# Kernel optimization log

Hardware: AMD Instinct MI355X
Metric: run time of the kernel (lower is better)

## Reference

```python
import jax, jax.numpy as jnp
import numpy as np

TOP_K = 2  # module default top_k


def setup_inputs() -> dict:
    key = jax.random.key(0)
    k1, k2, k3 = jax.random.split(key, 3)
    B, D, E = 4096, 1024, 64  # tokens, input_dim, num_experts
    return {
        "tensor1": jax.random.normal(k1, (B, D), dtype=jnp.float32),
        "tensor2": jax.random.normal(k2, (B, D), dtype=jnp.float32),
        "gate_weight": jax.random.normal(k3, (E, 2 * D), dtype=jnp.float32) * 0.02,
    }


def reference(tensor1, tensor2, gate_weight):
    # x: (B, 2D)
    x = jnp.concatenate((tensor1, tensor2), axis=-1)
    # pairwise L2 distance between each token and each expert vector
    diff = gate_weight[None, :, :] - x[:, None, :]          # (B, E, 2D)
    logits = -jnp.sqrt(jnp.sum(diff * diff, axis=-1))        # (B, E)
    topk_logits, indices = jax.lax.top_k(logits, TOP_K)      # (B, K)
    gating_weights = jax.nn.softmax(topk_logits, axis=-1)    # (B, K)
    rows = jnp.arange(logits.shape[0])[:, None]              # (B, 1)
    sparse_gating = jnp.zeros_like(logits).at[rows, indices].set(gating_weights)
    return sparse_gating
```

## Files before the change

kernel.cpp:

```cpp
#include <hip/hip_runtime.h>
#include <math.h>

#define NTOK 4096
#define NDIM 1024
#define KTOT 2048
#define NEXP 64
#define NKC  8
#define KCH  (KTOT / NKC)
#define NSTEP (KCH / 32)

typedef _Float16 half8 __attribute__((ext_vector_type(8)));
typedef float    floatx4 __attribute__((ext_vector_type(4)));

#define XSCALE 16.0f
#define WSCALE 1024.0f
#define INVSCALE (1.0f / (16.0f * 1024.0f))

struct h2pair { _Float16 h, l; };
__device__ __forceinline__ h2pair split2(float v) {
    h2pair r;
    r.h = (_Float16)v;
    r.l = (_Float16)(v - (float)r.h);
    return r;
}

__global__ __launch_bounds__(256) void prep_w(const float* __restrict__ W,
                                              _Float16* __restrict__ WhT,
                                              _Float16* __restrict__ WlT,
                                              float* __restrict__ nrm) {
    const int e = blockIdx.x, t = threadIdx.x;
    const float* row = W + (size_t)e * KTOT + t * 8;
    const float4 a = *reinterpret_cast<const float4*>(row);
    const float4 b = *reinterpret_cast<const float4*>(row + 4);
    float ss = fmaf(a.x, a.x, fmaf(a.y, a.y, fmaf(a.z, a.z, fmaf(a.w, a.w, 0.f))));
    ss = fmaf(b.x, b.x, fmaf(b.y, b.y, fmaf(b.z, b.z, fmaf(b.w, b.w, ss))));

    const h2pair p0 = split2(a.x * WSCALE), p1 = split2(a.y * WSCALE);
    const h2pair p2 = split2(a.z * WSCALE), p3 = split2(a.w * WSCALE);
    const h2pair p4 = split2(b.x * WSCALE), p5 = split2(b.y * WSCALE);
    const h2pair p6 = split2(b.z * WSCALE), p7 = split2(b.w * WSCALE);
    half8 h, l;
    h[0]=p0.h; h[1]=p1.h; h[2]=p2.h; h[3]=p3.h; h[4]=p4.h; h[5]=p5.h; h[6]=p6.h; h[7]=p7.h;
    l[0]=p0.l; l[1]=p1.l; l[2]=p2.l; l[3]=p3.l; l[4]=p4.l; l[5]=p5.l; l[6]=p6.l; l[7]=p7.l;
    const size_t idx = ((size_t)t * NEXP + e) * 8;
    *reinterpret_cast<half8*>(WhT + idx) = h;
    *reinterpret_cast<half8*>(WlT + idx) = l;

    #pragma unroll
    for (int off = 32; off > 0; off >>= 1) ss += __shfl_down(ss, off, 64);
    __shared__ float red[4];
    const int lane = t & 63, wv = t >> 6;
    if (lane == 0) red[wv] = ss;
    __syncthreads();
    if (t == 0) nrm[e] = (red[0] + red[1]) + (red[2] + red[3]);
}

__global__ __launch_bounds__(256) void gemm_frag(const float* __restrict__ t1,
                                                 const float* __restrict__ t2,
                                                 const _Float16* __restrict__ WhT,
                                                 const _Float16* __restrict__ WlT,
                                                 float* __restrict__ Gp,
                                                 float* __restrict__ Cp) {
    const int tid  = threadIdx.x;
    const int lane = tid & 63;
    const int gw   = blockIdx.x * 4 + (tid >> 6);
    const int tokg = gw >> 3;
    const int kc   = gw & 7;
    const int tok0 = tokg * 16;
    const int kbase = kc * KCH;
    const int n  = lane & 15;
    const int fq = lane >> 4;

    const float* __restrict__ xb = ((kbase < NDIM)
        ? (t1 + (size_t)(tok0 + n) * NDIM + kbase)
        : (t2 + (size_t)(tok0 + n) * NDIM + (kbase - NDIM))) + fq * 8;
    const _Float16* __restrict__ whb = WhT + ((size_t)(kbase >> 3) + fq) * (NEXP * 8) + n * 8;
    const _Float16* __restrict__ wlb = WlT + ((size_t)(kbase >> 3) + fq) * (NEXP * 8) + n * 8;

    floatx4 acc[4];
    #pragma unroll
    for (int j = 0; j < 4; ++j) { acc[j][0]=0.f; acc[j][1]=0.f; acc[j][2]=0.f; acc[j][3]=0.f; }
    float ssx = 0.f;

    #pragma unroll
    for (int s = 0; s < NSTEP; ++s) {
        const float4 x0 = *reinterpret_cast<const float4*>(xb + s * 32);
        const float4 x1 = *reinterpret_cast<const float4*>(xb + s * 32 + 4);
        half8 bh[4], bl[4];
        #pragma unroll
        for (int j = 0; j < 4; ++j) {
            bh[j] = *reinterpret_cast<const half8*>(whb + (size_t)s * 4 * (NEXP * 8) + j * 128);
            bl[j] = *reinterpret_cast<const half8*>(wlb + (size_t)s * 4 * (NEXP * 8) + j * 128);
        }
        ssx = fmaf(x0.x, x0.x, fmaf(x0.y, x0.y, fmaf(x0.z, x0.z, fmaf(x0.w, x0.w, ssx))));
        ssx = fmaf(x1.x, x1.x, fmaf(x1.y, x1.y, fmaf(x1.z, x1.z, fmaf(x1.w, x1.w, ssx))));
        const h2pair q0 = split2(x0.x * XSCALE), q1 = split2(x0.y * XSCALE);
        const h2pair q2 = split2(x0.z * XSCALE), q3 = split2(x0.w * XSCALE);
        const h2pair q4 = split2(x1.x * XSCALE), q5 = split2(x1.y * XSCALE);
        const h2pair q6 = split2(x1.z * XSCALE), q7 = split2(x1.w * XSCALE);
        half8 ah, al;
        ah[0]=q0.h; ah[1]=q1.h; ah[2]=q2.h; ah[3]=q3.h; ah[4]=q4.h; ah[5]=q5.h; ah[6]=q6.h; ah[7]=q7.h;
        al[0]=q0.l; al[1]=q1.l; al[2]=q2.l; al[3]=q3.l; al[4]=q4.l; al[5]=q5.l; al[6]=q6.l; al[7]=q7.l;
        #pragma unroll
        for (int j = 0; j < 4; ++j)
            acc[j] = __builtin_amdgcn_mfma_f32_16x16x32_f16(ah, bh[j], acc[j], 0, 0, 0);
        #pragma unroll
        for (int j = 0; j < 4; ++j)
            acc[j] = __builtin_amdgcn_mfma_f32_16x16x32_f16(al, bh[j], acc[j], 0, 0, 0);
        #pragma unroll
        for (int j = 0; j < 4; ++j)
            acc[j] = __builtin_amdgcn_mfma_f32_16x16x32_f16(ah, bl[j], acc[j], 0, 0, 0);
    }

    #pragma unroll
    for (int j = 0; j < 4; ++j) {
        #pragma unroll
        for (int i = 0; i < 4; ++i) {
            Gp[((size_t)kc * NTOK + tok0 + fq * 4 + i) * NEXP + 16 * j + n] = acc[j][i];
        }
    }

    ssx += __shfl_xor(ssx, 16, 64);
    ssx += __shfl_xor(ssx, 32, 64);
    if (lane < 16)
        Cp[(size_t)kc * NTOK + tok0 + lane] = ssx;
}

__global__ __launch_bounds__(256) void finalize(const float* __restrict__ Gp,
                                                const float* __restrict__ Cp,
                                                const float* __restrict__ nrm,
                                                float* __restrict__ out) {
    const int wv = threadIdx.x >> 6, lane = threadIdx.x & 63;
    const int token = blockIdx.x * 4 + wv;

    float gsum = 0.f, csum = 0.f;
    #pragma unroll
    for (int cix = 0; cix < NKC; ++cix) {
        gsum += Gp[((size_t)cix * NTOK + token) * NEXP + lane];
        csum += Cp[(size_t)cix * NTOK + token];
    }
    const float nv = nrm[lane];

    const float S = fmaf(-2.f * INVSCALE, gsum, csum) + nv;
    const float logit = -sqrtf(S);

    float v1 = logit; int i1 = lane;
    #pragma unroll
    for (int off = 32; off > 0; off >>= 1) {
        float ov = __shfl_xor(v1, off, 64);
        int   oi = __shfl_xor(i1, off, 64);
        if (ov > v1 || (ov == v1 && oi < i1)) { v1 = ov; i1 = oi; }
    }
    float v2 = (lane == i1) ? -__builtin_inff() : logit;
    int   i2 = lane;
    #pragma unroll
    for (int off = 32; off > 0; off >>= 1) {
        float ov = __shfl_xor(v2, off, 64);
        int   oi = __shfl_xor(i2, off, 64);
        if (ov > v2 || (ov == v2 && oi < i2)) { v2 = ov; i2 = oi; }
    }
    const float e2  = expf(v2 - v1);
    const float inv = 1.f / (1.f + e2);
    const float o = (lane == i1) ? inv : ((lane == i2) ? e2 * inv : 0.f);
    out[(size_t)token * NEXP + lane] = o;
}

extern "C" void kernel_launch(void* const* d_in, const int* in_sizes, int n_in,
                              void* d_out, int out_size, void* d_ws, size_t ws_size,
                              hipStream_t stream) {
    const float* t1 = (const float*)d_in[0];
    const float* t2 = (const float*)d_in[1];
    const float* W  = (const float*)d_in[2];
    float* out = (float*)d_out;

    char* ws = (char*)d_ws;
    float*    Gp  = (float*)ws;
    float*    Cp  = Gp + (size_t)NKC * NTOK * NEXP;
    float*    nrm = Cp + (size_t)NKC * NTOK;
    _Float16* WhT = (_Float16*)(nrm + NEXP);
    _Float16* WlT = WhT + (size_t)NEXP * KTOT;

    prep_w<<<NEXP, 256, 0, stream>>>(W, WhT, WlT, nrm);
    gemm_frag<<<(NTOK / 16) * NKC / 4, 256, 0, stream>>>(t1, t2, WhT, WlT, Gp, Cp);
    finalize<<<NTOK / 4, 256, 0, stream>>>(Gp, Cp, nrm, out);
}
```

Measured before the change: 89.96 us.

## Fuse split-K GEMM and top-k finalize into one kernel via LDS reduction

Merges the split-K fragment GEMM and the finalize kernel. Each 512-thread block now handles 16 tokens, with 8 waves each covering one K chunk. Partial dot products and norms go to shared memory (padded stride) instead of global workspace, then are reduced in-block before top-2 softmax. This removes the partial-sum global traffic (8x4096x64 floats written and re-read) and one kernel launch. In exchange the grid has fewer blocks (256), each carrying more LDS.

```diff
diff --git a/kernel.cpp b/kernel.cpp
--- a/kernel.cpp
+++ b/kernel.cpp
@@ -5,9 +5,10 @@
 #define NDIM 1024
 #define KTOT 2048
 #define NEXP 64
-#define NKC  8
-#define KCH  (KTOT / NKC)
+#define NWAVE 8
+#define KCH  (KTOT / NWAVE)
 #define NSTEP (KCH / 32)
+#define RS   68
 
 typedef _Float16 half8 __attribute__((ext_vector_type(8)));
 typedef float    floatx4 __attribute__((ext_vector_type(4)));
@@ -55,19 +56,20 @@
     if (t == 0) nrm[e] = (red[0] + red[1]) + (red[2] + red[3]);
 }
 
-__global__ __launch_bounds__(256) void gemm_frag(const float* __restrict__ t1,
-                                                 const float* __restrict__ t2,
-                                                 const _Float16* __restrict__ WhT,
-                                                 const _Float16* __restrict__ WlT,
-                                                 float* __restrict__ Gp,
-                                                 float* __restrict__ Cp) {
+__global__ __launch_bounds__(512) void gate_fused(const float* __restrict__ t1,
+                                                  const float* __restrict__ t2,
+                                                  const _Float16* __restrict__ WhT,
+                                                  const _Float16* __restrict__ WlT,
+                                                  const float* __restrict__ nrm,
+                                                  float* __restrict__ out) {
+    __shared__ float Sd[NWAVE][16 * RS];
+    __shared__ float Cn[NWAVE][16];
+
     const int tid  = threadIdx.x;
     const int lane = tid & 63;
-    const int gw   = blockIdx.x * 4 + (tid >> 6);
-    const int tokg = gw >> 3;
-    const int kc   = gw & 7;
-    const int tok0 = tokg * 16;
-    const int kbase = kc * KCH;
+    const int wv   = tid >> 6;
+    const int tok0 = blockIdx.x * 16;
+    const int kbase = wv * KCH;
     const int n  = lane & 15;
     const int fq = lane >> 4;
 
@@ -115,54 +117,46 @@
     #pragma unroll
     for (int j = 0; j < 4; ++j) {
         #pragma unroll
-        for (int i = 0; i < 4; ++i) {
-            Gp[((size_t)kc * NTOK + tok0 + fq * 4 + i) * NEXP + 16 * j + n] = acc[j][i];
-        }
+        for (int i = 0; i < 4; ++i)
+            Sd[wv][(fq * 4 + i) * RS + 16 * j + n] = acc[j][i];
     }
-
     ssx += __shfl_xor(ssx, 16, 64);
     ssx += __shfl_xor(ssx, 32, 64);
-    if (lane < 16)
-        Cp[(size_t)kc * NTOK + tok0 + lane] = ssx;
-}
+    if (lane < 16) Cn[wv][lane] = ssx;
+    __syncthreads();
 
-__global__ __launch_bounds__(256) void finalize(const float* __restrict__ Gp,
-                                                const float* __restrict__ Cp,
-                                                const float* __restrict__ nrm,
-                                                float* __restrict__ out) {
-    const int wv = threadIdx.x >> 6, lane = threadIdx.x & 63;
-    const int token = blockIdx.x * 4 + wv;
+    #pragma unroll
+    for (int tt = 0; tt < 2; ++tt) {
+        const int t = wv * 2 + tt;
+        float gsum = 0.f, csum = 0.f;
+        #pragma unroll
+        for (int w = 0; w < NWAVE; ++w) {
+            gsum += Sd[w][t * RS + lane];
+            csum += Cn[w][t];
+        }
+        const float S = fmaf(-2.f * INVSCALE, gsum, csum) + nrm[lane];
+        const float logit = -sqrtf(S);
 
-    float gsum = 0.f, csum = 0.f;
-    #pragma unroll
-    for (int cix = 0; cix < NKC; ++cix) {
-        gsum += Gp[((size_t)cix * NTOK + token) * NEXP + lane];
-        csum += Cp[(size_t)cix * NTOK + token];
+        float v1 = logit; int i1 = lane;
+        #pragma unroll
+        for (int off = 32; off > 0; off >>= 1) {
+            float ov = __shfl_xor(v1, off, 64);
+            int   oi = __shfl_xor(i1, off, 64);
+            if (ov > v1 || (ov == v1 && oi < i1)) { v1 = ov; i1 = oi; }
+        }
+        float v2 = (lane == i1) ? -__builtin_inff() : logit;
+        int   i2 = lane;
+        #pragma unroll
+        for (int off = 32; off > 0; off >>= 1) {
+            float ov = __shfl_xor(v2, off, 64);
+            int   oi = __shfl_xor(i2, off, 64);
+            if (ov > v2 || (ov == v2 && oi < i2)) { v2 = ov; i2 = oi; }
+        }
+        const float e2  = expf(v2 - v1);
+        const float inv = 1.f / (1.f + e2);
+        const float o = (lane == i1) ? inv : ((lane == i2) ? e2 * inv : 0.f);
+        out[(size_t)(tok0 + t) * NEXP + lane] = o;
     }
-    const float nv = nrm[lane];
-
-    const float S = fmaf(-2.f * INVSCALE, gsum, csum) + nv;
-    const float logit = -sqrtf(S);
-
-    float v1 = logit; int i1 = lane;
-    #pragma unroll
-    for (int off = 32; off > 0; off >>= 1) {
-        float ov = __shfl_xor(v1, off, 64);
-        int   oi = __shfl_xor(i1, off, 64);
-        if (ov > v1 || (ov == v1 && oi < i1)) { v1 = ov; i1 = oi; }
-    }
-    float v2 = (lane == i1) ? -__builtin_inff() : logit;
-    int   i2 = lane;
-    #pragma unroll
-    for (int off = 32; off > 0; off >>= 1) {
-        float ov = __shfl_xor(v2, off, 64);
-        int   oi = __shfl_xor(i2, off, 64);
-        if (ov > v2 || (ov == v2 && oi < i2)) { v2 = ov; i2 = oi; }
-    }
-    const float e2  = expf(v2 - v1);
-    const float inv = 1.f / (1.f + e2);
-    const float o = (lane == i1) ? inv : ((lane == i2) ? e2 * inv : 0.f);
-    out[(size_t)token * NEXP + lane] = o;
 }
 
 extern "C" void kernel_launch(void* const* d_in, const int* in_sizes, int n_in,
@@ -174,13 +168,10 @@
     float* out = (float*)d_out;
 
     char* ws = (char*)d_ws;
-    float*    Gp  = (float*)ws;
-    float*    Cp  = Gp + (size_t)NKC * NTOK * NEXP;
-    float*    nrm = Cp + (size_t)NKC * NTOK;
+    float*    nrm = (float*)ws;
     _Float16* WhT = (_Float16*)(nrm + NEXP);
     _Float16* WlT = WhT + (size_t)NEXP * KTOT;
 
     prep_w<<<NEXP, 256, 0, stream>>>(W, WhT, WlT, nrm);
-    gemm_frag<<<(NTOK / 16) * NKC / 4, 256, 0, stream>>>(t1, t2, WhT, WlT, Gp, Cp);
-    finalize<<<NTOK / 4, 256, 0, stream>>>(Gp, Cp, nrm, out);
+    gate_fused<<<NTOK / 16, 512, 0, stream>>>(t1, t2, WhT, WlT, nrm, out);
 }
```

After: 83.82 us. 1.07x faster.
